# Optimization experiments

Measured on AMD Instinct MI355X. Metric: run time of the kernel, lower is better.

The kernel has to match this reference:

```python
import jax, jax.numpy as jnp
import numpy as np
import math

TAU = 1.0  # init kwarg tau


def setup_inputs() -> dict:
    key = jax.random.key(0)
    n, m = 1024, 8192
    V = jax.random.normal(key, (n, m), dtype=jnp.float32)
    return {"V": V}


def reference(V) -> jnp.ndarray:
    n, m = V.shape
    num_rounds = math.ceil(m / n)
    # Repeat V row-blocks num_rounds times: M has shape [num_rounds*n, m]
    M = jnp.tile(V, (num_rounds, 1))

    def step(c, row):
        # Soft round-robin pick (training branch of SoftRR.__one_round)
        y = jax.nn.softmax((row - jnp.min(row) + 1.0) * c / TAU)
        c = (1.0 - y) * c
        return c, y

    c0 = jnp.ones((m,), dtype=V.dtype)
    _, R = jax.lax.scan(step, c0, M)  # R: [num_rounds*n, m]
    pi = R.reshape(num_rounds, n, m).sum(axis=0)  # [n, m]
    return pi
```

## Files before the change

kernel.cpp:

```cpp
#include <hip/hip_runtime.h>
#include <hip/hip_fp16.h>


#define N_ROWS 1024
#define M_COLS 8192
#define STEPS  8192
#define LOG2E  1.4426950408889634f

using half8  = __attribute__((ext_vector_type(8))) _Float16;
using half2v = __attribute__((ext_vector_type(2))) _Float16;
using f32x2  = __attribute__((ext_vector_type(2))) float;

__device__ __forceinline__ float fast_exp2(float x) {
#if __has_builtin(__builtin_amdgcn_exp2f)
  return __builtin_amdgcn_exp2f(x);
#else
  return exp2f(x);
#endif
}
__device__ __forceinline__ float fast_rcp(float x) {
#if __has_builtin(__builtin_amdgcn_rcpf)
  return __builtin_amdgcn_rcpf(x);
#else
  return 1.0f / x;
#endif
}
__device__ __forceinline__ half2v pack_f16(float y0, float y1) {
  return __builtin_bit_cast(half2v, __builtin_amdgcn_cvt_pkrtz(y0, y1));
}

template <int CTRL>
__device__ __forceinline__ float dpp_add(float x) {
  int yi = __builtin_amdgcn_update_dpp(0, __builtin_bit_cast(int, x),
                                       CTRL, 0xf, 0xf, true);
  return x + __builtin_bit_cast(float, yi);
}

__device__ __forceinline__ float wave_sum_to_lane63(float x) {
  x = dpp_add<0x111>(x);
  x = dpp_add<0x112>(x);
  x = dpp_add<0x114>(x);
  x = dpp_add<0x118>(x);
  x = dpp_add<0x142>(x);
  x = dpp_add<0x143>(x);
  return x;
}

#define BAR_LDS_ONLY() asm volatile("s_waitcnt lgkmcnt(0)\n\ts_barrier" ::: "memory")

__global__ void softrr_rowmin(const float* __restrict__ V, float* __restrict__ rmin) {
  const int row = blockIdx.x;
  const float* p = V + (size_t)row * M_COLS;
  float m = 1e30f;
  for (int j = threadIdx.x; j < M_COLS; j += 256) m = fminf(m, p[j]);
#pragma unroll
  for (int off = 32; off; off >>= 1) m = fminf(m, __shfl_xor(m, off, 64));
  __shared__ float sm[4];
  if ((threadIdx.x & 63) == 0) sm[threadIdx.x >> 6] = m;
  __syncthreads();
  if (threadIdx.x == 0) {
    rmin[row] = fminf(fminf(sm[0], sm[1]), fminf(sm[2], sm[3]));
  }
}

__global__ void softrr_prep(const float* __restrict__ V, const float* __restrict__ rmin,
                            __half* __restrict__ A) {
  const int idx8 = blockIdx.x * 256 + threadIdx.x;
  const int row = idx8 >> 10;
  const float mn = rmin[row];
  const float4* v4 = (const float4*)V;
  float4 va = v4[2 * idx8];
  float4 vb = v4[2 * idx8 + 1];
  half8 o;
  o[0] = (_Float16)((va.x - mn + 1.0f) * LOG2E);
  o[1] = (_Float16)((va.y - mn + 1.0f) * LOG2E);
  o[2] = (_Float16)((va.z - mn + 1.0f) * LOG2E);
  o[3] = (_Float16)((va.w - mn + 1.0f) * LOG2E);
  o[4] = (_Float16)((vb.x - mn + 1.0f) * LOG2E);
  o[5] = (_Float16)((vb.y - mn + 1.0f) * LOG2E);
  o[6] = (_Float16)((vb.z - mn + 1.0f) * LOG2E);
  o[7] = (_Float16)((vb.w - mn + 1.0f) * LOG2E);
  ((half8*)A)[idx8] = o;
}

__global__ void __launch_bounds__(512) softrr_scan_e(const __half* __restrict__ Ah,
                                                     __half* __restrict__ Eh,
                                                     float* __restrict__ SinvW) {
  const int t = threadIdx.x;
  const int wave = t >> 6;
  const int lane = t & 63;
  __shared__ float sP[2][8];

  const half8* __restrict__ A8 = (const half8*)Ah;
  half8* __restrict__ E8 = (half8*)Eh;

  f32x2 c[8];
#pragma unroll
  for (int k = 0; k < 8; ++k) c[k] = (f32x2){1.0f, 1.0f};

  half8 a0 = A8[2 * t];
  half8 a1 = A8[2 * t + 1];
  half8 b0 = A8[1024 + 2 * t];
  half8 b1 = A8[1024 + 2 * t + 1];

  for (int s = 0; s < STEPS; ++s) {
    const int ld  = (s + 2) & (N_ROWS - 1);
    const int par = s & 1;

    half8 n0 = A8[ld * 1024 + 2 * t];
    half8 n1 = A8[ld * 1024 + 2 * t + 1];

    f32x2 e[8];
#pragma unroll
    for (int k = 0; k < 4; ++k) {
      e[k][0]     = fast_exp2((float)a0[2 * k]     * c[k][0]);
      e[k][1]     = fast_exp2((float)a0[2 * k + 1] * c[k][1]);
      e[4 + k][0] = fast_exp2((float)a1[2 * k]     * c[4 + k][0]);
      e[4 + k][1] = fast_exp2((float)a1[2 * k + 1] * c[4 + k][1]);
    }

    f32x2 ce[8];
#pragma unroll
    for (int k = 0; k < 8; ++k) ce[k] = c[k] * e[k];

    half8 o0, o1;
#pragma unroll
    for (int k = 0; k < 4; ++k) {
      half2v h = pack_f16(e[k][0], e[k][1]);
      o0[2 * k] = h[0]; o0[2 * k + 1] = h[1];
      half2v g = pack_f16(e[4 + k][0], e[4 + k][1]);
      o1[2 * k] = g[0]; o1[2 * k + 1] = g[1];
    }
    E8[(size_t)s * 1024 + 2 * t]     = o0;
    E8[(size_t)s * 1024 + 2 * t + 1] = o1;

    f32x2 t0 = (e[0] + e[1]) + (e[2] + e[3]);
    f32x2 t1 = (e[4] + e[5]) + (e[6] + e[7]);
    f32x2 tw = t0 + t1;
    float l = tw[0] + tw[1];

    l = wave_sum_to_lane63(l);
    if (lane == 63) sP[par][wave] = l;
    BAR_LDS_ONLY();

    float x = (lane < 8) ? sP[par][lane] : 0.0f;
    x = dpp_add<0x111>(x);
    x = dpp_add<0x112>(x);
    x = dpp_add<0x114>(x);
    const float S = __builtin_bit_cast(
        float, __builtin_amdgcn_readlane(__builtin_bit_cast(int, x), 7));
    const float Sinv = fast_rcp(S);
    if (t == 0) SinvW[s] = Sinv;

    const f32x2 Sv = (f32x2){Sinv, Sinv};
#pragma unroll
    for (int k = 0; k < 8; ++k) c[k] = c[k] - ce[k] * Sv;

    a0 = b0; a1 = b1;
    b0 = n0; b1 = n1;
  }
}

__global__ void softrr_sum8s(const __half* __restrict__ Eh,
                             const float* __restrict__ SinvW,
                             float* __restrict__ out) {
  const int idx8 = blockIdx.x * 256 + threadIdx.x;
  const int i = idx8 >> 10;
  const int w = idx8 & 1023;
  const half8* E8 = (const half8*)Eh;

  float si[8];
#pragma unroll
  for (int r = 0; r < 8; ++r) si[r] = SinvW[r * 1024 + i];

  float acc[8];
#pragma unroll
  for (int k = 0; k < 8; ++k) acc[k] = 0.0f;
#pragma unroll
  for (int r = 0; r < 8; ++r) {
    half8 v = E8[(size_t)(r * 1024 + i) * 1024 + w];
#pragma unroll
    for (int k = 0; k < 8; ++k) acc[k] = __builtin_fmaf((float)v[k], si[r], acc[k]);
  }
  ((float4*)out)[2 * idx8]     = make_float4(acc[0], acc[1], acc[2], acc[3]);
  ((float4*)out)[2 * idx8 + 1] = make_float4(acc[4], acc[5], acc[6], acc[7]);
}

__global__ void __launch_bounds__(1024) softrr_scan_b(const float* __restrict__ V,
                                                      const float* __restrict__ rmin,
                                                      float* __restrict__ out) {
  const int t = threadIdx.x;
  const int wave = t >> 6;
  const int lane = t & 63;
  __shared__ float partials[2][16];
  __shared__ float smin[N_ROWS];
  smin[t] = rmin[t];
  __syncthreads();
  const float4* __restrict__ V4 = (const float4*)V;
  float4* O4 = (float4*)out;
  float c[8];
#pragma unroll
  for (int k = 0; k < 8; ++k) c[k] = 1.0f;
  float4 va = V4[2 * t], vb = V4[2 * t + 1];
  float4 pa, pb;
  for (int s = 0; s < STEPS; ++s) {
    const int i = s & (N_ROWS - 1);
    const int r = s >> 10;
    const int in_ = (s + 1) & (N_ROWS - 1);
    float4 van = V4[in_ * 2048 + 2 * t];
    float4 vbn = V4[in_ * 2048 + 2 * t + 1];
    const float mn = smin[i];
    const float base = (1.0f - mn) * LOG2E;
    float vv[8] = {va.x, va.y, va.z, va.w, vb.x, vb.y, vb.z, vb.w};
    float e[8];
    float l = 0.0f;
#pragma unroll
    for (int k = 0; k < 8; ++k) {
      float zb = __builtin_fmaf(vv[k], LOG2E, base);
      e[k] = fast_exp2(zb * c[k]);
      l += e[k];
    }
#pragma unroll
    for (int off = 32; off; off >>= 1) l += __shfl_xor(l, off, 64);
    if (lane == 0) partials[s & 1][wave] = l;
    __syncthreads();
    float S = 0.0f;
#pragma unroll
    for (int w = 0; w < 16; ++w) S += partials[s & 1][w];
    const float Sinv = fast_rcp(S);
    float po[8] = {pa.x, pa.y, pa.z, pa.w, pb.x, pb.y, pb.z, pb.w};
    float o[8];
#pragma unroll
    for (int k = 0; k < 8; ++k) {
      float y = e[k] * Sinv;
      c[k] = __builtin_fmaf(-y, c[k], c[k]);
      o[k] = (r > 0) ? (po[k] + y) : y;
    }
    O4[i * 2048 + 2 * t]     = make_float4(o[0], o[1], o[2], o[3]);
    O4[i * 2048 + 2 * t + 1] = make_float4(o[4], o[5], o[6], o[7]);
    va = van; vb = vbn;
    pa = O4[in_ * 2048 + 2 * t];
    pb = O4[in_ * 2048 + 2 * t + 1];
  }
}

extern "C" void kernel_launch(void* const* d_in, const int* in_sizes, int n_in,
                              void* d_out, int out_size, void* d_ws, size_t ws_size,
                              hipStream_t stream) {
  const float* V = (const float*)d_in[0];
  float* out = (float*)d_out;
  float* rmin = (float*)d_ws;

  const size_t E_BYTES = (size_t)STEPS * M_COLS * 2;
  const size_t S_BYTES = (size_t)STEPS * 4;
  const size_t need = 4096 + E_BYTES + S_BYTES;

  if (ws_size >= need) {
    __half* A    = (__half*)out;
    __half* E    = (__half*)((char*)d_ws + 4096);
    float*  Sinv = (float*)((char*)d_ws + 4096 + E_BYTES);
    softrr_rowmin<<<N_ROWS, 256, 0, stream>>>(V, rmin);
    softrr_prep<<<4096, 256, 0, stream>>>(V, rmin, A);
    softrr_scan_e<<<1, 512, 0, stream>>>(A, E, Sinv);
    softrr_sum8s<<<4096, 256, 0, stream>>>(E, Sinv, out);
  } else {
    softrr_rowmin<<<N_ROWS, 256, 0, stream>>>(V, rmin);
    softrr_scan_b<<<1, 1024, 0, stream>>>(V, rmin, out);
  }
}
```

Baseline: 5.149 ms.

## Run serial scan with 4 waves and permuted column layout for coalesced loads

The single-block sequential scan drops from 512 to 256 threads, so each thread now owns 32 columns. The prep and final-sum kernels permute the column layout so each thread's half8 loads and stores stay coalesced as q*256+t. The step loop is unrolled by two with separate X/Y register buffers that prefetch two steps ahead. The cross-wave reduction becomes a single float4 LDS read. The aim is cheaper barriers and reduction per step in this latency-bound scan, at the cost of doubling the per-thread exp and ALU work on the critical path.

```diff
diff --git a/kernel.cpp b/kernel.cpp
--- a/kernel.cpp
+++ b/kernel.cpp
@@ -63,14 +63,18 @@
   }
 }
 
-__global__ void softrr_prep(const float* __restrict__ V, const float* __restrict__ rmin,
-                            __half* __restrict__ A) {
-  const int idx8 = blockIdx.x * 256 + threadIdx.x;
-  const int row = idx8 >> 10;
+__global__ void softrr_prep_perm(const float* __restrict__ V, const float* __restrict__ rmin,
+                                 __half* __restrict__ A) {
+  const int gid = blockIdx.x * 256 + threadIdx.x;
+  const int row = gid >> 10;
+  const int pc  = gid & 1023;
+  const int q   = pc >> 8;
+  const int tt  = pc & 255;
+  const int cc  = 4 * tt + q;
   const float mn = rmin[row];
-  const float4* v4 = (const float4*)V;
-  float4 va = v4[2 * idx8];
-  float4 vb = v4[2 * idx8 + 1];
+  const float4* V4 = (const float4*)V;
+  float4 va = V4[row * 2048 + 2 * cc];
+  float4 vb = V4[row * 2048 + 2 * cc + 1];
   half8 o;
   o[0] = (_Float16)((va.x - mn + 1.0f) * LOG2E);
   o[1] = (_Float16)((va.y - mn + 1.0f) * LOG2E);
@@ -80,93 +84,101 @@
   o[5] = (_Float16)((vb.y - mn + 1.0f) * LOG2E);
   o[6] = (_Float16)((vb.z - mn + 1.0f) * LOG2E);
   o[7] = (_Float16)((vb.w - mn + 1.0f) * LOG2E);
-  ((half8*)A)[idx8] = o;
-}
-
-__global__ void __launch_bounds__(512) softrr_scan_e(const __half* __restrict__ Ah,
-                                                     __half* __restrict__ Eh,
-                                                     float* __restrict__ SinvW) {
+  ((half8*)A)[gid] = o;
+}
+
+__global__ void __launch_bounds__(256) softrr_scan4(const __half* __restrict__ Ah,
+                                                    __half* __restrict__ Eh,
+                                                    float* __restrict__ SinvW) {
   const int t = threadIdx.x;
   const int wave = t >> 6;
   const int lane = t & 63;
-  __shared__ float sP[2][8];
+  __shared__ __align__(16) float sP[2][4];
 
   const half8* __restrict__ A8 = (const half8*)Ah;
   half8* __restrict__ E8 = (half8*)Eh;
 
-  f32x2 c[8];
-#pragma unroll
-  for (int k = 0; k < 8; ++k) c[k] = (f32x2){1.0f, 1.0f};
-
-  half8 a0 = A8[2 * t];
-  half8 a1 = A8[2 * t + 1];
-  half8 b0 = A8[1024 + 2 * t];
-  half8 b1 = A8[1024 + 2 * t + 1];
-
-  for (int s = 0; s < STEPS; ++s) {
-    const int ld  = (s + 2) & (N_ROWS - 1);
-    const int par = s & 1;
-
-    half8 n0 = A8[ld * 1024 + 2 * t];
-    half8 n1 = A8[ld * 1024 + 2 * t + 1];
-
-    f32x2 e[8];
-#pragma unroll
-    for (int k = 0; k < 4; ++k) {
-      e[k][0]     = fast_exp2((float)a0[2 * k]     * c[k][0]);
-      e[k][1]     = fast_exp2((float)a0[2 * k + 1] * c[k][1]);
-      e[4 + k][0] = fast_exp2((float)a1[2 * k]     * c[4 + k][0]);
-      e[4 + k][1] = fast_exp2((float)a1[2 * k + 1] * c[4 + k][1]);
-    }
-
-    f32x2 ce[8];
-#pragma unroll
-    for (int k = 0; k < 8; ++k) ce[k] = c[k] * e[k];
-
-    half8 o0, o1;
-#pragma unroll
-    for (int k = 0; k < 4; ++k) {
-      half2v h = pack_f16(e[k][0], e[k][1]);
-      o0[2 * k] = h[0]; o0[2 * k + 1] = h[1];
-      half2v g = pack_f16(e[4 + k][0], e[4 + k][1]);
-      o1[2 * k] = g[0]; o1[2 * k + 1] = g[1];
-    }
-    E8[(size_t)s * 1024 + 2 * t]     = o0;
-    E8[(size_t)s * 1024 + 2 * t + 1] = o1;
-
-    f32x2 t0 = (e[0] + e[1]) + (e[2] + e[3]);
-    f32x2 t1 = (e[4] + e[5]) + (e[6] + e[7]);
-    f32x2 tw = t0 + t1;
+  f32x2 c[16];
+#pragma unroll
+  for (int k = 0; k < 16; ++k) c[k] = (f32x2){1.0f, 1.0f};
+
+  half8 X[4], Y[4];
+#pragma unroll
+  for (int q = 0; q < 4; ++q) X[q] = A8[q * 256 + t];
+#pragma unroll
+  for (int q = 0; q < 4; ++q) Y[q] = A8[1024 + q * 256 + t];
+
+  unsigned aoffE = 2 * 1024, aoffO = 3 * 1024;
+  unsigned eoffE = 0,        eoffO = 1024;
+
+  auto half_step = [&](half8 (&B)[4], unsigned aoff, unsigned eoff, int par, int s) {
+    f32x2 e[16];
+#pragma unroll
+    for (int q = 0; q < 4; ++q) {
+#pragma unroll
+      for (int j = 0; j < 4; ++j) {
+        const int k = q * 4 + j;
+        e[k][0] = fast_exp2((float)B[q][2 * j]     * c[k][0]);
+        e[k][1] = fast_exp2((float)B[q][2 * j + 1] * c[k][1]);
+      }
+    }
+#pragma unroll
+    for (int q = 0; q < 4; ++q) B[q] = A8[aoff + q * 256 + t];
+
+#pragma unroll
+    for (int q = 0; q < 4; ++q) {
+      half8 o;
+#pragma unroll
+      for (int j = 0; j < 4; ++j) {
+        half2v h = pack_f16(e[q * 4 + j][0], e[q * 4 + j][1]);
+        o[2 * j] = h[0]; o[2 * j + 1] = h[1];
+      }
+      E8[eoff + q * 256 + t] = o;
+    }
+
+    f32x2 u0 = (e[0] + e[1]) + (e[2] + e[3]);
+    f32x2 u1 = (e[4] + e[5]) + (e[6] + e[7]);
+    f32x2 u2 = (e[8] + e[9]) + (e[10] + e[11]);
+    f32x2 u3 = (e[12] + e[13]) + (e[14] + e[15]);
+    f32x2 tw = (u0 + u1) + (u2 + u3);
     float l = tw[0] + tw[1];
 
     l = wave_sum_to_lane63(l);
     if (lane == 63) sP[par][wave] = l;
     BAR_LDS_ONLY();
 
-    float x = (lane < 8) ? sP[par][lane] : 0.0f;
-    x = dpp_add<0x111>(x);
-    x = dpp_add<0x112>(x);
-    x = dpp_add<0x114>(x);
-    const float S = __builtin_bit_cast(
-        float, __builtin_amdgcn_readlane(__builtin_bit_cast(int, x), 7));
+    float4 p4 = *(const float4*)(&sP[par][0]);
+    const float S = (p4.x + p4.y) + (p4.z + p4.w);
     const float Sinv = fast_rcp(S);
     if (t == 0) SinvW[s] = Sinv;
 
     const f32x2 Sv = (f32x2){Sinv, Sinv};
 #pragma unroll
-    for (int k = 0; k < 8; ++k) c[k] = c[k] - ce[k] * Sv;
-
-    a0 = b0; a1 = b1;
-    b0 = n0; b1 = n1;
-  }
-}
-
-__global__ void softrr_sum8s(const __half* __restrict__ Eh,
+    for (int k = 0; k < 16; ++k) {
+      e[k] = c[k] * e[k];
+      c[k] = c[k] - e[k] * Sv;
+    }
+  };
+
+  for (int s = 0; s < STEPS; s += 2) {
+    half_step(X, aoffE, eoffE, 0, s);
+    aoffE = (aoffE + 2048) & (1024 * 1024 - 1);
+    eoffE += 2048;
+    half_step(Y, aoffO, eoffO, 1, s + 1);
+    aoffO = (aoffO + 2048) & (1024 * 1024 - 1);
+    eoffO += 2048;
+  }
+}
+
+__global__ void softrr_sum8p(const __half* __restrict__ Eh,
                              const float* __restrict__ SinvW,
                              float* __restrict__ out) {
-  const int idx8 = blockIdx.x * 256 + threadIdx.x;
-  const int i = idx8 >> 10;
-  const int w = idx8 & 1023;
+  const int gid = blockIdx.x * 256 + threadIdx.x;
+  const int i  = gid >> 10;
+  const int pc = gid & 1023;
+  const int q  = pc >> 8;
+  const int tt = pc & 255;
+  const int cc = 4 * tt + q;
   const half8* E8 = (const half8*)Eh;
 
   float si[8];
@@ -178,12 +190,12 @@
   for (int k = 0; k < 8; ++k) acc[k] = 0.0f;
 #pragma unroll
   for (int r = 0; r < 8; ++r) {
-    half8 v = E8[(size_t)(r * 1024 + i) * 1024 + w];
+    half8 v = E8[(size_t)(r * 1024 + i) * 1024 + pc];
 #pragma unroll
     for (int k = 0; k < 8; ++k) acc[k] = __builtin_fmaf((float)v[k], si[r], acc[k]);
   }
-  ((float4*)out)[2 * idx8]     = make_float4(acc[0], acc[1], acc[2], acc[3]);
-  ((float4*)out)[2 * idx8 + 1] = make_float4(acc[4], acc[5], acc[6], acc[7]);
+  ((float4*)out)[(size_t)i * 2048 + 2 * cc]     = make_float4(acc[0], acc[1], acc[2], acc[3]);
+  ((float4*)out)[(size_t)i * 2048 + 2 * cc + 1] = make_float4(acc[4], acc[5], acc[6], acc[7]);
 }
 
 __global__ void __launch_bounds__(1024) softrr_scan_b(const float* __restrict__ V,
@@ -260,9 +272,9 @@
     __half* E    = (__half*)((char*)d_ws + 4096);
     float*  Sinv = (float*)((char*)d_ws + 4096 + E_BYTES);
     softrr_rowmin<<<N_ROWS, 256, 0, stream>>>(V, rmin);
-    softrr_prep<<<4096, 256, 0, stream>>>(V, rmin, A);
-    softrr_scan_e<<<1, 512, 0, stream>>>(A, E, Sinv);
-    softrr_sum8s<<<4096, 256, 0, stream>>>(E, Sinv, out);
+    softrr_prep_perm<<<4096, 256, 0, stream>>>(V, rmin, A);
+    softrr_scan4<<<1, 256, 0, stream>>>(A, E, Sinv);
+    softrr_sum8p<<<4096, 256, 0, stream>>>(E, Sinv, out);
   } else {
     softrr_rowmin<<<N_ROWS, 256, 0, stream>>>(V, rmin);
     softrr_scan_b<<<1, 1024, 0, stream>>>(V, rmin, out);
```

Result: faster. 5.012 ms (-2.7%).

## Split sequential scan across 16 single-wave blocks synced via global atomics

Applied to the files above, without the earlier changes.

Replaces the single 512-thread block scan with 16 one-wave blocks, each owning 512 columns. The blocks exchange per-step partial softmax denominators through a packed fixed-point 64-bit atomic counter in global memory and spin until all 16 have arrived. This aims to spread the exp work over more compute units and cut per-wave register pressure. In exchange, each of the 8192 steps now pays a device-scope atomic and polling round trip, and the fixed-point encoding slightly quantizes the sums.

```diff
diff --git a/kernel.cpp b/kernel.cpp
--- a/kernel.cpp
+++ b/kernel.cpp
@@ -6,6 +6,8 @@
 #define M_COLS 8192
 #define STEPS  8192
 #define LOG2E  1.4426950408889634f
+#define NWAVE  16
+#define FXS    1048576.0f
 
 using half8  = __attribute__((ext_vector_type(8))) _Float16;
 using half2v = __attribute__((ext_vector_type(2))) _Float16;
@@ -45,8 +47,6 @@
   x = dpp_add<0x143>(x);
   return x;
 }
-
-#define BAR_LDS_ONLY() asm volatile("s_waitcnt lgkmcnt(0)\n\ts_barrier" ::: "memory")
 
 __global__ void softrr_rowmin(const float* __restrict__ V, float* __restrict__ rmin) {
   const int row = blockIdx.x;
@@ -83,81 +83,73 @@
   ((half8*)A)[idx8] = o;
 }
 
-__global__ void __launch_bounds__(512) softrr_scan_e(const __half* __restrict__ Ah,
-                                                     __half* __restrict__ Eh,
-                                                     float* __restrict__ SinvW) {
-  const int t = threadIdx.x;
-  const int wave = t >> 6;
-  const int lane = t & 63;
-  __shared__ float sP[2][8];
+__global__ void softrr_zero(unsigned long long* __restrict__ Sync) {
+  Sync[blockIdx.x * 256 + threadIdx.x] = 0ULL;
+}
+
+__global__ void __launch_bounds__(64) softrr_scan_g(const __half* __restrict__ Ah,
+                                                    __half* __restrict__ Eh,
+                                                    float* __restrict__ SinvW,
+                                                    unsigned long long* __restrict__ Sync) {
+  const int w    = blockIdx.x;
+  const int lane = threadIdx.x;
+  const int base = 64 * w + lane;
 
   const half8* __restrict__ A8 = (const half8*)Ah;
   half8* __restrict__ E8 = (half8*)Eh;
 
-  f32x2 c[8];
-#pragma unroll
-  for (int k = 0; k < 8; ++k) c[k] = (f32x2){1.0f, 1.0f};
-
-  half8 a0 = A8[2 * t];
-  half8 a1 = A8[2 * t + 1];
-  half8 b0 = A8[1024 + 2 * t];
-  half8 b1 = A8[1024 + 2 * t + 1];
-
-  for (int s = 0; s < STEPS; ++s) {
-    const int ld  = (s + 2) & (N_ROWS - 1);
-    const int par = s & 1;
-
-    half8 n0 = A8[ld * 1024 + 2 * t];
-    half8 n1 = A8[ld * 1024 + 2 * t + 1];
-
-    f32x2 e[8];
-#pragma unroll
-    for (int k = 0; k < 4; ++k) {
-      e[k][0]     = fast_exp2((float)a0[2 * k]     * c[k][0]);
-      e[k][1]     = fast_exp2((float)a0[2 * k + 1] * c[k][1]);
-      e[4 + k][0] = fast_exp2((float)a1[2 * k]     * c[4 + k][0]);
-      e[4 + k][1] = fast_exp2((float)a1[2 * k + 1] * c[4 + k][1]);
-    }
-
-    f32x2 ce[8];
-#pragma unroll
-    for (int k = 0; k < 8; ++k) ce[k] = c[k] * e[k];
-
-    half8 o0, o1;
-#pragma unroll
-    for (int k = 0; k < 4; ++k) {
-      half2v h = pack_f16(e[k][0], e[k][1]);
-      o0[2 * k] = h[0]; o0[2 * k + 1] = h[1];
-      half2v g = pack_f16(e[4 + k][0], e[4 + k][1]);
-      o1[2 * k] = g[0]; o1[2 * k + 1] = g[1];
-    }
-    E8[(size_t)s * 1024 + 2 * t]     = o0;
-    E8[(size_t)s * 1024 + 2 * t + 1] = o1;
-
-    f32x2 t0 = (e[0] + e[1]) + (e[2] + e[3]);
-    f32x2 t1 = (e[4] + e[5]) + (e[6] + e[7]);
-    f32x2 tw = t0 + t1;
-    float l = tw[0] + tw[1];
-
+  f32x2 c[4];
+#pragma unroll
+  for (int k = 0; k < 4; ++k) c[k] = (f32x2){1.0f, 1.0f};
+
+  half8 X = A8[base];
+  half8 Y = A8[1024 + base];
+
+  auto half_step = [&](half8& B, int s) {
+    f32x2 e[4];
+#pragma unroll
+    for (int j = 0; j < 4; ++j) {
+      e[j][0] = fast_exp2((float)B[2 * j]     * c[j][0]);
+      e[j][1] = fast_exp2((float)B[2 * j + 1] * c[j][1]);
+    }
+    B = A8[((s + 2) & (N_ROWS - 1)) * 1024 + base];
+
+    half8 o;
+#pragma unroll
+    for (int j = 0; j < 4; ++j) {
+      half2v h = pack_f16(e[j][0], e[j][1]);
+      o[2 * j] = h[0]; o[2 * j + 1] = h[1];
+    }
+    E8[(size_t)s * 1024 + base] = o;
+
+    f32x2 u = (e[0] + e[1]) + (e[2] + e[3]);
+    float l = u[0] + u[1];
     l = wave_sum_to_lane63(l);
-    if (lane == 63) sP[par][wave] = l;
-    BAR_LDS_ONLY();
-
-    float x = (lane < 8) ? sP[par][lane] : 0.0f;
-    x = dpp_add<0x111>(x);
-    x = dpp_add<0x112>(x);
-    x = dpp_add<0x114>(x);
-    const float S = __builtin_bit_cast(
-        float, __builtin_amdgcn_readlane(__builtin_bit_cast(int, x), 7));
+
+    if (lane == 63) {
+      unsigned long long pk = (1ULL << 56) | (unsigned long long)(l * FXS);
+      __hip_atomic_fetch_add(&Sync[s], pk, __ATOMIC_RELAXED, __HIP_MEMORY_SCOPE_AGENT);
+    }
+    unsigned long long v;
+    do {
+      v = __hip_atomic_load(&Sync[s], __ATOMIC_RELAXED, __HIP_MEMORY_SCOPE_AGENT);
+    } while ((v >> 56) != (unsigned long long)NWAVE);
+
+    const float S = (float)(v & 0x00FFFFFFFFFFFFFFULL) * (1.0f / FXS);
     const float Sinv = fast_rcp(S);
-    if (t == 0) SinvW[s] = Sinv;
+    if (w == 0 && lane == 0) SinvW[s] = Sinv;
 
     const f32x2 Sv = (f32x2){Sinv, Sinv};
 #pragma unroll
-    for (int k = 0; k < 8; ++k) c[k] = c[k] - ce[k] * Sv;
-
-    a0 = b0; a1 = b1;
-    b0 = n0; b1 = n1;
+    for (int j = 0; j < 4; ++j) {
+      e[j] = c[j] * e[j];
+      c[j] = c[j] - e[j] * Sv;
+    }
+  };
+
+  for (int s = 0; s < STEPS; s += 2) {
+    half_step(X, s);
+    half_step(Y, s + 1);
   }
 }
 
@@ -226,7 +218,7 @@
     __syncthreads();
     float S = 0.0f;
 #pragma unroll
-    for (int w = 0; w < 16; ++w) S += partials[s & 1][w];
+    for (int ww = 0; ww < 16; ++ww) S += partials[s & 1][ww];
     const float Sinv = fast_rcp(S);
     float po[8] = {pa.x, pa.y, pa.z, pa.w, pb.x, pb.y, pb.z, pb.w};
     float o[8];
@@ -251,17 +243,21 @@
   float* out = (float*)d_out;
   float* rmin = (float*)d_ws;
 
-  const size_t E_BYTES = (size_t)STEPS * M_COLS * 2;
-  const size_t S_BYTES = (size_t)STEPS * 4;
-  const size_t need = 4096 + E_BYTES + S_BYTES;
+  const size_t E_BYTES  = (size_t)STEPS * M_COLS * 2;
+  const size_t S_BYTES  = (size_t)STEPS * 4;
+  const size_t SY_BYTES = (size_t)STEPS * 8;
+  const size_t need = 4096 + E_BYTES + S_BYTES + SY_BYTES;
 
   if (ws_size >= need) {
     __half* A    = (__half*)out;
     __half* E    = (__half*)((char*)d_ws + 4096);
     float*  Sinv = (float*)((char*)d_ws + 4096 + E_BYTES);
+    unsigned long long* Sync =
+        (unsigned long long*)((char*)d_ws + 4096 + E_BYTES + S_BYTES);
     softrr_rowmin<<<N_ROWS, 256, 0, stream>>>(V, rmin);
     softrr_prep<<<4096, 256, 0, stream>>>(V, rmin, A);
-    softrr_scan_e<<<1, 512, 0, stream>>>(A, E, Sinv);
+    softrr_zero<<<STEPS / 256, 256, 0, stream>>>(Sync);
+    softrr_scan_g<<<NWAVE, 64, 0, stream>>>(A, E, Sinv, Sync);
     softrr_sum8s<<<4096, 256, 0, stream>>>(E, Sinv, out);
   } else {
     softrr_rowmin<<<N_ROWS, 256, 0, stream>>>(V, rmin);
```

Measured after the change: 8.225 ms. 1.6x slower.
